# Kernel tuning notes

Hardware: AMD Instinct MI355X
Metric: run time of the kernel (lower is better)

Reference implementation:

```python
import jax, jax.numpy as jnp
import numpy as np

jax.config.update("jax_enable_x64", True)

B, H, W = 16384, 19, 19
MAX_FLOOD = min(H * W // 4, 100)  # = 90, as in the torch module


def _count_neighbors(m):
    # m: [B,H,W] float. Sum of 4 orthogonal neighbors (zero-padded edges).
    up = jnp.pad(m[:, :-1, :], ((0, 0), (1, 0), (0, 0)))
    down = jnp.pad(m[:, 1:, :], ((0, 0), (0, 1), (0, 0)))
    left = jnp.pad(m[:, :, :-1], ((0, 0), (0, 0), (1, 0)))
    right = jnp.pad(m[:, :, 1:], ((0, 0), (0, 0), (0, 1)))
    return up + down + left + right


def _dilate(m):
    # m: [B,H,W] bool. OR of 4 orthogonal neighbors (False-padded edges).
    up = jnp.pad(m[:, :-1, :], ((0, 0), (1, 0), (0, 0)))
    down = jnp.pad(m[:, 1:, :], ((0, 0), (0, 1), (0, 0)))
    left = jnp.pad(m[:, :, :-1], ((0, 0), (0, 0), (1, 0)))
    right = jnp.pad(m[:, :, 1:], ((0, 0), (0, 0), (0, 1)))
    return up | down | left | right


def _flood_fill(seeds, mask):
    # Iterative neighbor expansion within mask, bounded iters + early exit.
    def cond(st):
        _, changed, i = st
        return changed & (i < MAX_FLOOD)

    def body(st):
        g, _, i = st
        exp = _dilate(g) & mask & ~g
        return (g | exp, exp.any(), i + 1)

    g, _, _ = jax.lax.while_loop(cond, body, (seeds, seeds.any(), jnp.int32(0)))
    return g


def setup_inputs() -> dict:
    key = jax.random.key(0)
    k1, k2, k3, k4, k5, k6 = jax.random.split(key, 6)
    # 0 = empty, 1 = black, 2 = white (planes never overlap)
    board = jax.random.randint(k1, (B, H, W), 0, 3)
    stones = jnp.stack([board == 1, board == 2], axis=1).astype(jnp.float32)
    current_player = jax.random.randint(k2, (B,), 0, 2).astype(jnp.int32)
    ko_rc = jax.random.randint(k3, (B, 2), 0, H).astype(jnp.int32)
    has_ko = jax.random.uniform(k4, (B,)) < 0.25
    ko_points = jnp.where(has_ko[:, None], ko_rc, jnp.int32(-1))
    hmax = np.iinfo(np.int64).max
    zobrist_stones = jax.random.randint(k5, (2, H, W), 0, hmax, dtype=jnp.int64)
    zobrist_turn = jax.random.randint(k6, (2,), 0, hmax, dtype=jnp.int64)
    position_hash = jnp.zeros((B,), jnp.int64)
    return {
        "stones": stones,
        "current_player": current_player,
        "ko_points": ko_points,
        "zobrist_stones": zobrist_stones,
        "zobrist_turn": zobrist_turn,
        "position_hash": position_hash,
    }


def reference(stones, current_player, ko_points, zobrist_stones, zobrist_turn, position_hash):
    stones_b = stones > 0.5                       # [B,2,H,W] bool
    empty_f = 1.0 - stones.sum(axis=1)            # [B,H,W] float (0/1)
    empty = ~stones_b.any(axis=1)                 # empty_mask
    liberties = _count_neighbors(empty_f)         # float liberty count per point

    # legal = empty points with at least one empty neighbor
    legal = empty & (liberties > 0.0)

    # capture moves: opponent stones with exactly one liberty
    cp = current_player.astype(jnp.int32)
    opp = jnp.take_along_axis(stones_b, (1 - cp)[:, None, None, None], axis=1)[:, 0]
    vulnerable = opp & (jnp.round(liberties).astype(jnp.int32) == 1)
    cap = empty & (_count_neighbors(vulnerable.astype(jnp.float32)) > 0.0)
    legal = legal | cap

    # ko restriction: mask the single ko point per game (if set)
    valid_ko = ko_points[:, 0] >= 0
    r_eq = jnp.arange(H)[None, :, None] == ko_points[:, 0][:, None, None]
    c_eq = jnp.arange(W)[None, None, :] == ko_points[:, 1][:, None, None]
    legal = legal & ~(valid_ko[:, None, None] & r_eq & c_eq)

    # flood fill the full groups-in-atari within opponent stones
    groups = _flood_fill(vulnerable, opp)

    # zobrist hash: XOR of stone hashes over the board + turn toggle
    contrib = jnp.where(stones_b, zobrist_stones[None], jnp.int64(0))  # [B,2,H,W]
    board_hash = jax.lax.reduce(contrib, np.int64(0), jax.lax.bitwise_xor, (1, 2, 3))
    new_hash = position_hash ^ board_hash ^ zobrist_turn[cp] ^ zobrist_turn[1 - cp]

    return (liberties, legal, groups, new_hash)
```

## Files before the change

kernel.cpp:

```cpp
#include <hip/hip_runtime.h>
#include <stdint.h>

#define WW 19
#define NP 361
#define M19 0x7FFFFu
#define BPW 3
#define NWAVES 4
#define BPB (BPW * NWAVES)
#define TPB 256
#define BBSTR 25
#define PLSTR 97

__device__ __forceinline__ uint32_t rev19(uint32_t x) { return __brev(x) >> 13; }

__device__ __forceinline__ uint32_t runfill(uint32_t g, uint32_t m) {
  const uint32_t up = g | (m & ((m + g) ^ m ^ g));
  const uint32_t rm = rev19(m);
  const uint32_t rg = rev19(g);
  const uint32_t dn = rg | (rm & ((rm + rg) ^ rm ^ rg));
  return up | rev19(dn);
}

__global__ __launch_bounds__(TPB, 4) void go_fused(
    const float* __restrict__ stones, const int* __restrict__ cur,
    const int* __restrict__ ko, const int* __restrict__ zob,
    const int* __restrict__ zturn, const int* __restrict__ phash,
    float* __restrict__ out, int B) {
  __shared__ uint32_t bbuf[BPB * BBSTR];
  __shared__ uint32_t pl[BPB * PLSTR];

  const int wid = threadIdx.x >> 6;
  const int lane = threadIdx.x & 63;
  const int b0 = blockIdx.x * BPB;
  const size_t NB = (size_t)B * NP;

  int zb[6], zw[6];
#pragma unroll
  for (int i = 0; i < 6; ++i) {
    const int p = i * 64 + lane;
    zb[i] = (p < NP) ? zob[p] : 0;
    zw[i] = (p < NP) ? zob[NP + p] : 0;
  }
  const int zt = zturn[0] ^ zturn[1];

  int acc[BPW];
#pragma unroll
  for (int k = 0; k < BPW; ++k) {
    const int lb = wid * BPW + k;
    const int b = b0 + lb;
    acc[k] = 0;
    if (b < B) {
      const float* sb = stones + (size_t)b * (2 * NP);
#pragma unroll
      for (int i = 0; i < 6; ++i) {
        const int p = i * 64 + lane;
        const bool inb = p < NP;
        const float bv = inb ? sb[p] : 0.0f;
        const float wv = inb ? sb[NP + p] : 0.0f;
        const bool bs = bv > 0.5f, wsn = wv > 0.5f;
        const uint64_t bbm = __ballot(bs);
        const uint64_t wbm = __ballot(wsn);
        if (lane < 4) {
          const uint64_t src = (lane < 2) ? bbm : wbm;
          const uint32_t vv = (lane & 1) ? (uint32_t)(src >> 32) : (uint32_t)src;
          bbuf[lb * BBSTR + i * 4 + lane] = vv;
        }
        acc[k] ^= zb[i] & (bs ? -1 : 0);
        acc[k] ^= zw[i] & (wsn ? -1 : 0);
      }
    }
  }
#pragma unroll
  for (int off = 32; off > 0; off >>= 1) {
#pragma unroll
    for (int k = 0; k < BPW; ++k) acc[k] ^= __shfl_xor(acc[k], off, 64);
  }
  if (lane == 0) {
#pragma unroll
    for (int k = 0; k < BPW; ++k) {
      const int b = b0 + wid * BPW + k;
      if (b < B) out[3 * NB + b] = (float)(phash[b] ^ acc[k] ^ zt);
    }
  }
  __syncthreads();

  {
    const int k = (lane * 27) >> 9;
    const int r = lane - k * WW;
    const int lb = wid * BPW + k;
    const int b = b0 + lb;
    const bool vl = (lane < 57) && (b < B);
    const int lbs = vl ? lb : 0;
    const int bsafe = vl ? b : (B - 1);

    const int cp = cur[bsafe];
    const int2 kk = ((const int2*)ko)[bsafe];

    uint32_t mrow, erow;
    {
      const int bit = WW * r;
      const int w = bit >> 6, sh = bit & 63;
      const uint32_t* q = &bbuf[lbs * BBSTR + 4 * w];
      const uint64_t Blo = (uint64_t)q[0] | ((uint64_t)q[1] << 32);
      const uint64_t Wlo = (uint64_t)q[2] | ((uint64_t)q[3] << 32);
      uint32_t br = (uint32_t)(Blo >> sh);
      uint32_t wr = (uint32_t)(Wlo >> sh);
      if (sh > 45) {
        const uint64_t Bhi = (uint64_t)q[4] | ((uint64_t)q[5] << 32);
        const uint64_t Whi = (uint64_t)q[6] | ((uint64_t)q[7] << 32);
        br |= (uint32_t)(Bhi << (64 - sh));
        wr |= (uint32_t)(Whi << (64 - sh));
      }
      br &= M19;
      wr &= M19;
      mrow = vl ? ((cp == 0) ? wr : br) : 0u;
      erow = vl ? (~(br | wr) & M19) : 0u;
    }

    uint32_t t;
    t = __shfl(erow, lane - 1, 64);
    const uint32_t eu = (r > 0) ? t : 0u;
    t = __shfl(erow, lane + 1, 64);
    const uint32_t ed = (r < 18) ? t : 0u;
    const uint32_t el = (erow << 1) & M19;
    const uint32_t er_ = erow >> 1;
    const uint32_t s1 = eu ^ ed, c1 = eu & ed;
    const uint32_t s2 = el ^ er_, c2 = el & er_;
    const uint32_t cc = s1 & s2;
    const uint32_t L0 = s1 ^ s2;
    const uint32_t L1 = c1 ^ c2 ^ cc;
    const uint32_t L2 = (c1 & c2) | (cc & (c1 | c2));
    uint32_t leg = erow & (eu | ed | el | er_);
    const uint32_t vul = mrow & L0 & ~L1;
    t = __shfl(vul, lane - 1, 64);
    const uint32_t vu = (r > 0) ? t : 0u;
    t = __shfl(vul, lane + 1, 64);
    const uint32_t vd = (r < 18) ? t : 0u;
    leg |= erow & (vu | vd | ((vul << 1) & M19) | (vul >> 1));
    if (kk.x == r) leg &= ~(1u << kk.y);

    uint32_t g = runfill(vul, mrow);
    for (int it = 0; it < 90; ++it) {
      t = __shfl(g, lane - 1, 64);
      const uint32_t gu = (r > 0) ? t : 0u;
      t = __shfl(g, lane + 1, 64);
      const uint32_t gd = (r < 18) ? t : 0u;
      const uint32_t gn = runfill(g | ((gu | gd) & mrow), mrow);
      if (!__any(gn != g)) break;
      g = gn;
    }

    if (vl) {
      uint32_t* pb = &pl[lb * PLSTR];
      pb[r] = L0;
      pb[19 + r] = L1;
      pb[38 + r] = L2;
      pb[57 + r] = leg;
      pb[76 + r] = g;
    }
  }
  __syncthreads();

  if (b0 + BPB <= B) {
    float4* s0 = (float4*)(out + (size_t)b0 * NP);
    float4* s1 = (float4*)(out + NB + (size_t)b0 * NP);
    float4* s2 = (float4*)(out + 2 * NB + (size_t)b0 * NP);
    const int nq = BPB * NP / 4;
    for (int q = threadIdx.x; q < nq; q += TPB) {
      float t0[4], t1[4], t2[4];
#pragma unroll
      for (int j = 0; j < 4; ++j) {
        const int id = q * 4 + j;
        const int lb = (id * 92949) >> 25;
        const int p = id - lb * NP;
        const int r = (p * 27) >> 9;
        const int c = p - r * WW;
        const uint32_t* pb = &pl[lb * PLSTR];
        const uint32_t l0 = (pb[r] >> c) & 1u;
        const uint32_t l1 = (pb[19 + r] >> c) & 1u;
        const uint32_t l2 = (pb[38 + r] >> c) & 1u;
        t0[j] = (float)(l0 + 2u * l1 + 4u * l2);
        t1[j] = (float)((pb[57 + r] >> c) & 1u);
        t2[j] = (float)((pb[76 + r] >> c) & 1u);
      }
      s0[q] = make_float4(t0[0], t0[1], t0[2], t0[3]);
      s1[q] = make_float4(t1[0], t1[1], t1[2], t1[3]);
      s2[q] = make_float4(t2[0], t2[1], t2[2], t2[3]);
    }
  } else {
#pragma unroll
    for (int k = 0; k < BPW; ++k) {
      const int lb = wid * BPW + k;
      const int b = b0 + lb;
      if (b < B) {
        float* o0 = out + (size_t)b * NP;
        const uint32_t* pb = &pl[lb * PLSTR];
#pragma unroll
        for (int i = 0; i < 6; ++i) {
          const int p = i * 64 + lane;
          if (p < NP) {
            const int r = (p * 27) >> 9;
            const int c = p - r * WW;
            const uint32_t l0 = (pb[r] >> c) & 1u;
            const uint32_t l1 = (pb[19 + r] >> c) & 1u;
            const uint32_t l2 = (pb[38 + r] >> c) & 1u;
            o0[p] = (float)(l0 + 2u * l1 + 4u * l2);
            o0[NB + p] = (float)((pb[57 + r] >> c) & 1u);
            o0[2 * NB + p] = (float)((pb[76 + r] >> c) & 1u);
          }
        }
      }
    }
  }
}

extern "C" void kernel_launch(void* const* d_in, const int* in_sizes, int n_in,
                              void* d_out, int out_size, void* d_ws,
                              size_t ws_size, hipStream_t stream) {
  const float* stones = (const float*)d_in[0];
  const int* cur = (const int*)d_in[1];
  const int* ko = (const int*)d_in[2];
  const int* zob = (const int*)d_in[3];
  const int* zturn = (const int*)d_in[4];
  const int* phash = (const int*)d_in[5];
  float* out = (float*)d_out;

  const int B = in_sizes[0] / (2 * NP);
  const int blocks = (B + BPB - 1) / BPB;
  go_fused<<<blocks, TPB, 0, stream>>>(stones, cur, ko, zob, zturn, phash, out,
                                       B);
}
```

Before: 29.76 us.

## Load stones as contiguous float4 chunks into a packed shared bitmap

```diff
diff --git a/kernel.cpp b/kernel.cpp
--- a/kernel.cpp
+++ b/kernel.cpp
@@ -5,11 +5,15 @@
 #define NP 361
 #define M19 0x7FFFFu
 #define BPW 3
-#define NWAVES 4
-#define BPB (BPW * NWAVES)
-#define TPB 256
-#define BBSTR 25
+#define NWAVES 8
+#define BPB 24
+#define TPB 512
+#define CHF (BPB * 722)
+#define CH4 (CHF / 4)
+#define BMW 548
 #define PLSTR 97
+
+typedef float f32x4 __attribute__((ext_vector_type(4)));
 
 __device__ __forceinline__ uint32_t rev19(uint32_t x) { return __brev(x) >> 13; }
 
@@ -21,18 +25,21 @@
   return up | rev19(dn);
 }
 
-__global__ __launch_bounds__(TPB, 4) void go_fused(
+__global__ __launch_bounds__(TPB, 2) void go_fused(
     const float* __restrict__ stones, const int* __restrict__ cur,
     const int* __restrict__ ko, const int* __restrict__ zob,
     const int* __restrict__ zturn, const int* __restrict__ phash,
     float* __restrict__ out, int B) {
-  __shared__ uint32_t bbuf[BPB * BBSTR];
+  __shared__ uint32_t bmp[BMW];
   __shared__ uint32_t pl[BPB * PLSTR];
 
   const int wid = threadIdx.x >> 6;
   const int lane = threadIdx.x & 63;
   const int b0 = blockIdx.x * BPB;
+  const int nb = min(BPB, B - b0);
   const size_t NB = (size_t)B * NP;
+
+  for (int t = threadIdx.x; t < BMW; t += TPB) bmp[t] = 0;
 
   int zb[6], zw[6];
 #pragma unroll
@@ -42,80 +49,88 @@
     zw[i] = (p < NP) ? zob[NP + p] : 0;
   }
   const int zt = zturn[0] ^ zturn[1];
-
-  int acc[BPW];
-#pragma unroll
-  for (int k = 0; k < BPW; ++k) {
-    const int lb = wid * BPW + k;
-    const int b = b0 + lb;
-    acc[k] = 0;
-    if (b < B) {
-      const float* sb = stones + (size_t)b * (2 * NP);
+  __syncthreads();
+
+  {
+    const f32x4* src = (const f32x4*)(stones + (size_t)b0 * 722);
+    const int nf4 = nb * 722 / 4;
+#pragma unroll
+    for (int j = 0; j < (CH4 + TPB - 1) / TPB; ++j) {
+      const int q = threadIdx.x + TPB * j;
+      uint32_t m = 0;
+      if (q < nf4) {
+        const f32x4 v = __builtin_nontemporal_load(&src[q]);
+        m = (uint32_t)(v.x > 0.5f) | ((uint32_t)(v.y > 0.5f) << 1) |
+            ((uint32_t)(v.z > 0.5f) << 2) | ((uint32_t)(v.w > 0.5f) << 3);
+      }
+      uint32_t x = m | ((uint32_t)__shfl_xor((int)m, 1, 64) << 4);
+      x = x | ((uint32_t)__shfl_xor((int)x, 2, 64) << 8);
+      x = x | ((uint32_t)__shfl_xor((int)x, 4, 64) << 16);
+      if ((lane & 7) == 0 && q < CH4) bmp[q >> 3] = x;
+    }
+  }
+  __syncthreads();
+
+  {
+    int hv[BPW];
+#pragma unroll
+    for (int k = 0; k < BPW; ++k) {
+      const int lb = wid * BPW + k;
+      const uint32_t base = lb * 722;
+      int h = 0;
 #pragma unroll
       for (int i = 0; i < 6; ++i) {
-        const int p = i * 64 + lane;
-        const bool inb = p < NP;
-        const float bv = inb ? sb[p] : 0.0f;
-        const float wv = inb ? sb[NP + p] : 0.0f;
-        const bool bs = bv > 0.5f, wsn = wv > 0.5f;
-        const uint64_t bbm = __ballot(bs);
-        const uint64_t wbm = __ballot(wsn);
-        if (lane < 4) {
-          const uint64_t src = (lane < 2) ? bbm : wbm;
-          const uint32_t vv = (lane & 1) ? (uint32_t)(src >> 32) : (uint32_t)src;
-          bbuf[lb * BBSTR + i * 4 + lane] = vv;
+        const int cc = i * 64 + lane;
+        if (cc < NP) {
+          uint32_t pos = base + cc;
+          uint32_t s = (bmp[pos >> 5] >> (pos & 31)) & 1u;
+          h ^= zb[i] & -(int)s;
+          pos = base + 361 + cc;
+          s = (bmp[pos >> 5] >> (pos & 31)) & 1u;
+          h ^= zw[i] & -(int)s;
         }
-        acc[k] ^= zb[i] & (bs ? -1 : 0);
-        acc[k] ^= zw[i] & (wsn ? -1 : 0);
-      }
-    }
-  }
-#pragma unroll
-  for (int off = 32; off > 0; off >>= 1) {
-#pragma unroll
-    for (int k = 0; k < BPW; ++k) acc[k] ^= __shfl_xor(acc[k], off, 64);
-  }
-  if (lane == 0) {
-#pragma unroll
-    for (int k = 0; k < BPW; ++k) {
-      const int b = b0 + wid * BPW + k;
-      if (b < B) out[3 * NB + b] = (float)(phash[b] ^ acc[k] ^ zt);
-    }
-  }
-  __syncthreads();
+      }
+      hv[k] = h;
+    }
+#pragma unroll
+    for (int off = 32; off > 0; off >>= 1) {
+#pragma unroll
+      for (int k = 0; k < BPW; ++k) hv[k] ^= __shfl_xor(hv[k], off, 64);
+    }
+    if (lane == 0) {
+#pragma unroll
+      for (int k = 0; k < BPW; ++k) {
+        const int b = b0 + wid * BPW + k;
+        if (b < B) out[3 * NB + b] = (float)(phash[b] ^ hv[k] ^ zt);
+      }
+    }
+  }
 
   {
     const int k = (lane * 27) >> 9;
     const int r = lane - k * WW;
     const int lb = wid * BPW + k;
     const int b = b0 + lb;
-    const bool vl = (lane < 57) && (b < B);
+    const bool vl = (lane < 57) && (lb < nb);
     const int lbs = vl ? lb : 0;
-    const int bsafe = vl ? b : (B - 1);
-
-    const int cp = cur[bsafe];
-    const int2 kk = ((const int2*)ko)[bsafe];
-
-    uint32_t mrow, erow;
+
+    uint32_t brow, wrow;
     {
-      const int bit = WW * r;
-      const int w = bit >> 6, sh = bit & 63;
-      const uint32_t* q = &bbuf[lbs * BBSTR + 4 * w];
-      const uint64_t Blo = (uint64_t)q[0] | ((uint64_t)q[1] << 32);
-      const uint64_t Wlo = (uint64_t)q[2] | ((uint64_t)q[3] << 32);
-      uint32_t br = (uint32_t)(Blo >> sh);
-      uint32_t wr = (uint32_t)(Wlo >> sh);
-      if (sh > 45) {
-        const uint64_t Bhi = (uint64_t)q[4] | ((uint64_t)q[5] << 32);
-        const uint64_t Whi = (uint64_t)q[6] | ((uint64_t)q[7] << 32);
-        br |= (uint32_t)(Bhi << (64 - sh));
-        wr |= (uint32_t)(Whi << (64 - sh));
-      }
-      br &= M19;
-      wr &= M19;
-      mrow = vl ? ((cp == 0) ? wr : br) : 0u;
-      erow = vl ? (~(br | wr) & M19) : 0u;
-    }
+      const uint32_t base = (uint32_t)lbs * 722 + (uint32_t)r * WW;
+      const uint32_t d = base >> 5, sh = base & 31;
+      const uint64_t w = ((uint64_t)bmp[d + 1] << 32) | bmp[d];
+      brow = (uint32_t)(w >> sh) & M19;
+      const uint32_t base2 = base + 361;
+      const uint32_t d2 = base2 >> 5, sh2 = base2 & 31;
+      const uint64_t w2 = ((uint64_t)bmp[d2 + 1] << 32) | bmp[d2];
+      wrow = (uint32_t)(w2 >> sh2) & M19;
+    }
+    const int cp = vl ? cur[b] : 0;
+    int2 kk = {-1, -1};
+    if (vl) kk = ((const int2*)ko)[b];
+    uint32_t mrow = (cp == 0) ? wrow : brow;
+    uint32_t erow = ~(brow | wrow) & M19;
+    if (!vl) { mrow = 0; erow = 0; }
 
     uint32_t t;
     t = __shfl(erow, lane - 1, 64);
@@ -161,17 +176,17 @@
   }
   __syncthreads();
 
-  if (b0 + BPB <= B) {
-    float4* s0 = (float4*)(out + (size_t)b0 * NP);
-    float4* s1 = (float4*)(out + NB + (size_t)b0 * NP);
-    float4* s2 = (float4*)(out + 2 * NB + (size_t)b0 * NP);
-    const int nq = BPB * NP / 4;
+  {
+    const int nq = nb * NP / 4;
+    f32x4* s0 = (f32x4*)(out + (size_t)b0 * NP);
+    f32x4* s1 = (f32x4*)(out + NB + (size_t)b0 * NP);
+    f32x4* s2 = (f32x4*)(out + 2 * NB + (size_t)b0 * NP);
     for (int q = threadIdx.x; q < nq; q += TPB) {
-      float t0[4], t1[4], t2[4];
+      f32x4 t0, t1, t2;
 #pragma unroll
       for (int j = 0; j < 4; ++j) {
         const int id = q * 4 + j;
-        const int lb = (id * 92949) >> 25;
+        const int lb = (int)(((uint64_t)id * 5948986ull) >> 31);
         const int p = id - lb * NP;
         const int r = (p * 27) >> 9;
         const int c = p - r * WW;
@@ -183,33 +198,23 @@
         t1[j] = (float)((pb[57 + r] >> c) & 1u);
         t2[j] = (float)((pb[76 + r] >> c) & 1u);
       }
-      s0[q] = make_float4(t0[0], t0[1], t0[2], t0[3]);
-      s1[q] = make_float4(t1[0], t1[1], t1[2], t1[3]);
-      s2[q] = make_float4(t2[0], t2[1], t2[2], t2[3]);
-    }
-  } else {
-#pragma unroll
-    for (int k = 0; k < BPW; ++k) {
-      const int lb = wid * BPW + k;
-      const int b = b0 + lb;
-      if (b < B) {
-        float* o0 = out + (size_t)b * NP;
-        const uint32_t* pb = &pl[lb * PLSTR];
-#pragma unroll
-        for (int i = 0; i < 6; ++i) {
-          const int p = i * 64 + lane;
-          if (p < NP) {
-            const int r = (p * 27) >> 9;
-            const int c = p - r * WW;
-            const uint32_t l0 = (pb[r] >> c) & 1u;
-            const uint32_t l1 = (pb[19 + r] >> c) & 1u;
-            const uint32_t l2 = (pb[38 + r] >> c) & 1u;
-            o0[p] = (float)(l0 + 2u * l1 + 4u * l2);
-            o0[NB + p] = (float)((pb[57 + r] >> c) & 1u);
-            o0[2 * NB + p] = (float)((pb[76 + r] >> c) & 1u);
-          }
-        }
-      }
+      __builtin_nontemporal_store(t0, &s0[q]);
+      __builtin_nontemporal_store(t1, &s1[q]);
+      __builtin_nontemporal_store(t2, &s2[q]);
+    }
+    const int rem0 = nq * 4;
+    for (int id = rem0 + threadIdx.x; id < nb * NP; id += TPB) {
+      const int lb = (int)(((uint64_t)id * 5948986ull) >> 31);
+      const int p = id - lb * NP;
+      const int r = (p * 27) >> 9;
+      const int c = p - r * WW;
+      const uint32_t* pb = &pl[lb * PLSTR];
+      const uint32_t l0 = (pb[r] >> c) & 1u;
+      const uint32_t l1 = (pb[19 + r] >> c) & 1u;
+      const uint32_t l2 = (pb[38 + r] >> c) & 1u;
+      out[(size_t)b0 * NP + id] = (float)(l0 + 2u * l1 + 4u * l2);
+      out[NB + (size_t)b0 * NP + id] = (float)((pb[57 + r] >> c) & 1u);
+      out[2 * NB + (size_t)b0 * NP + id] = (float)((pb[76 + r] >> c) & 1u);
     }
   }
 }
```

After: 29.59 us. Within noise of the previous version (-0.6%).
